# Optimization experiments

Hardware: AMD Instinct MI355X
Metric: run time of the kernel (lower is better)

Reference implementation:

```python
import jax, jax.numpy as jnp
import numpy as np


def setup_inputs() -> dict:
    key = jax.random.key(0)
    ks = jax.random.split(key, 4)
    N, T, D, H = 64, 512, 1024, 1024
    x = jax.random.normal(ks[0], (N, T, D), dtype=jnp.float32)
    h0 = jax.random.normal(ks[1], (N, H), dtype=jnp.float32)
    Wx = jax.random.normal(ks[2], (D, 4 * H), dtype=jnp.float32) / np.sqrt(D)
    Wh = jax.random.normal(ks[3], (H, 4 * H), dtype=jnp.float32) / np.sqrt(H)
    b = jnp.zeros((4 * H,), dtype=jnp.float32)
    return {"x": x, "h0": h0, "Wx": Wx, "Wh": Wh, "b": b}


def reference(x, h0, Wx, Wh, b):
    # x: [N, T, D]; h0: [N, H]; Wx: [D, 4H]; Wh: [H, 4H]; b: [4H]
    H = h0.shape[1]
    # Batch the input-to-hidden matmul over all timesteps at once: [N, T, 4H]
    xW = jnp.einsum('ntd,df->ntf', x, Wx) + b
    c0 = jnp.zeros_like(h0)

    def step(carry, xw_t):
        prev_h, prev_c = carry
        preact = xw_t + prev_h @ Wh           # [N, 4H]
        ai, af, ao, ag = jnp.split(preact, 4, axis=1)
        i = jax.nn.sigmoid(ai)
        f = jax.nn.sigmoid(af)
        o = jax.nn.sigmoid(ao)
        g = jnp.tanh(ag)
        next_c = f * prev_c + i * g
        next_h = o * jnp.tanh(next_c)
        return (next_h, next_c), next_h

    # scan over time: move T to leading axis
    _, hs = jax.lax.scan(step, (h0, c0), jnp.swapaxes(xW, 0, 1))
    return jnp.swapaxes(hs, 0, 1)  # [N, T, H]
```

## Files before the change

kernel.cpp:

```cpp
#include <hip/hip_runtime.h>
#include <cstdint>
#include <cstddef>

#define N_ 64
#define T_ 512
#define D_ 1024
#define H_ 1024
#define FH 4096

typedef __attribute__((ext_vector_type(8))) short bf16x8;
typedef __attribute__((ext_vector_type(4))) float f32x4;

static __device__ __forceinline__ uint16_t f2bf_(float f) {
  union { float f; uint32_t u; } v; v.f = f;
  uint32_t u = v.u + 0x7FFFu + ((v.u >> 16) & 1u);
  return (uint16_t)(u >> 16);
}
static __device__ __forceinline__ float bf2f_(uint16_t s) {
  union { uint32_t u; float f; } v; v.u = ((uint32_t)s) << 16;
  return v.f;
}
static __device__ __forceinline__ void unpk2_(unsigned long long e,
                                              uint32_t& hi, uint32_t& lo) {
  uint32_t a = (uint32_t)e, b = (uint32_t)(e >> 32);
  hi = (a >> 16) | (b & 0xFFFF0000u);
  lo = (a & 0xFFFFu) | (b << 16);
}

#define ALD(p) (*(p))

__global__ __launch_bounds__(256) void pack_w_k(const float* __restrict__ W,
                                                ushort* __restrict__ hi,
                                                ushort* __restrict__ lo) {
  const int i = blockIdx.x * 256 + threadIdx.x;
  const int lane = i & 63, kc = (i >> 6) & 31, bid = i >> 11;
  const int c = lane & 15;
  const int col = (c >> 2) * H_ + (bid << 2) + (c & 3);
  const int k0 = (kc << 5) + ((lane >> 4) << 3);
  const size_t o = ((size_t)(bid * 32 + kc) * 64 + lane) * 8;
#pragma unroll
  for (int e = 0; e < 8; ++e) {
    float v = W[(size_t)(k0 + e) * FH + col];
    ushort h = f2bf_(v);
    hi[o + e] = h;
    lo[o + e] = f2bf_(v - bf2f_(h));
  }
}

__global__ __launch_bounds__(256) void split_f32_k(const float* __restrict__ src,
                                                   ushort* __restrict__ hi,
                                                   ushort* __restrict__ lo,
                                                   unsigned* bar) {
  if (bar != nullptr && blockIdx.x == 0) {
    bar[threadIdx.x] = 0u;
    bar[256 + threadIdx.x] = 0u;
  }
  const size_t i = (size_t)blockIdx.x * 256 + threadIdx.x;
  float4 v = reinterpret_cast<const float4*>(src)[i];
  ushort4 h, l;
  h.x = f2bf_(v.x); l.x = f2bf_(v.x - bf2f_(h.x));
  h.y = f2bf_(v.y); l.y = f2bf_(v.y - bf2f_(h.y));
  h.z = f2bf_(v.z); l.z = f2bf_(v.z - bf2f_(h.z));
  h.w = f2bf_(v.w); l.w = f2bf_(v.w - bf2f_(h.w));
  reinterpret_cast<ushort4*>(hi)[i] = h;
  reinterpret_cast<ushort4*>(lo)[i] = l;
}

__global__ __launch_bounds__(256) void conv_h0pk_k(const float* __restrict__ src,
                                                   uint32_t* __restrict__ dst) {
  const int i = blockIdx.x * 256 + threadIdx.x;
  float4 v = reinterpret_cast<const float4*>(src)[i];
  uint4 o;
  { ushort h = f2bf_(v.x); o.x = ((uint32_t)h << 16) | f2bf_(v.x - bf2f_(h)); }
  { ushort h = f2bf_(v.y); o.y = ((uint32_t)h << 16) | f2bf_(v.y - bf2f_(h)); }
  { ushort h = f2bf_(v.z); o.z = ((uint32_t)h << 16) | f2bf_(v.z - bf2f_(h)); }
  { ushort h = f2bf_(v.w); o.w = ((uint32_t)h << 16) | f2bf_(v.w - bf2f_(h)); }
  reinterpret_cast<uint4*>(dst)[i] = o;
}

__global__ __launch_bounds__(512, 2) void lstm_persist_mfma(
    const ushort* __restrict__ Whh_g, const ushort* __restrict__ Whl_g,
    const ushort* __restrict__ Wxh, const ushort* __restrict__ Wxl,
    const ushort* __restrict__ xh, const ushort* __restrict__ xl,
    const float* __restrict__ bias,
    uint32_t* __restrict__ hseq,
    float* __restrict__ out, unsigned* __restrict__ bar) {
  extern __shared__ char ldsraw[];
  bf16x8* const WhH = (bf16x8*)ldsraw;
  bf16x8* const WhL = WhH + 2048;
  float* const pre = (float*)(WhL + 2048);
  float (*const xwr)[64][4][4] =
      (float(*)[64][4][4])(pre + 64 * 17);

  const int tid = threadIdx.x, bid = blockIdx.x;
  const int lane = tid & 63, w = tid >> 6;
  const int mt = w & 3;
  const int arow = (mt << 4) | (lane & 15);
  const int kg = lane >> 4;
  const int dc = lane & 15, dr = (lane >> 4) << 2;
  const int en = tid >> 2, ejj = tid & 3;

  unsigned* const rel = bar + 384;

  float bias4[4] = {0.f, 0.f, 0.f, 0.f};
  float creg = 0.f;
  if (tid < 256) {
#pragma unroll
    for (int g = 0; g < 4; ++g) bias4[g] = bias[g * H_ + (bid << 2) + ejj];
  }

  {
    const bf16x8* gh = reinterpret_cast<const bf16x8*>(Whh_g) + (size_t)bid * 2048;
    const bf16x8* gl = reinterpret_cast<const bf16x8*>(Whl_g) + (size_t)bid * 2048;
#pragma unroll
    for (int r = 0; r < 4; ++r) {
      int u = tid + (r << 9);
      WhH[u] = gh[u];
      WhL[u] = gl[u];
    }
  }
  __syncthreads();

  const bf16x8* Bxh = reinterpret_cast<const bf16x8*>(Wxh) + (size_t)bid * 2048 + lane;
  const bf16x8* Bxl = reinterpret_cast<const bf16x8*>(Wxl) + (size_t)bid * 2048 + lane;

  auto xburst = [&](int tb) {
    f32x4 xa0 = {0.f, 0.f, 0.f, 0.f};
    f32x4 xa1 = {0.f, 0.f, 0.f, 0.f};
    f32x4 xa2 = {0.f, 0.f, 0.f, 0.f};
    f32x4 xa3 = {0.f, 0.f, 0.f, 0.f};
    const ushort* axh = xh + ((size_t)arow * T_ + tb) * D_ + (kg << 3);
    const ushort* axl = xl + ((size_t)arow * T_ + tb) * D_ + (kg << 3);
#pragma unroll 4
    for (int kc = 0; kc < 32; ++kc) {
      bf16x8 bh = Bxh[kc << 6];
      bf16x8 bl = Bxl[kc << 6];
      bf16x8 a0h = *reinterpret_cast<const bf16x8*>(axh + (kc << 5));
      bf16x8 a0l = *reinterpret_cast<const bf16x8*>(axl + (kc << 5));
      bf16x8 a1h = *reinterpret_cast<const bf16x8*>(axh + D_ + (kc << 5));
      bf16x8 a1l = *reinterpret_cast<const bf16x8*>(axl + D_ + (kc << 5));
      bf16x8 a2h = *reinterpret_cast<const bf16x8*>(axh + 2 * D_ + (kc << 5));
      bf16x8 a2l = *reinterpret_cast<const bf16x8*>(axl + 2 * D_ + (kc << 5));
      bf16x8 a3h = *reinterpret_cast<const bf16x8*>(axh + 3 * D_ + (kc << 5));
      bf16x8 a3l = *reinterpret_cast<const bf16x8*>(axl + 3 * D_ + (kc << 5));
      xa0 = __builtin_amdgcn_mfma_f32_16x16x32_bf16(a0h, bh, xa0, 0, 0, 0);
      xa1 = __builtin_amdgcn_mfma_f32_16x16x32_bf16(a1h, bh, xa1, 0, 0, 0);
      xa2 = __builtin_amdgcn_mfma_f32_16x16x32_bf16(a2h, bh, xa2, 0, 0, 0);
      xa3 = __builtin_amdgcn_mfma_f32_16x16x32_bf16(a3h, bh, xa3, 0, 0, 0);
      xa0 = __builtin_amdgcn_mfma_f32_16x16x32_bf16(a0h, bl, xa0, 0, 0, 0);
      xa1 = __builtin_amdgcn_mfma_f32_16x16x32_bf16(a1h, bl, xa1, 0, 0, 0);
      xa2 = __builtin_amdgcn_mfma_f32_16x16x32_bf16(a2h, bl, xa2, 0, 0, 0);
      xa3 = __builtin_amdgcn_mfma_f32_16x16x32_bf16(a3h, bl, xa3, 0, 0, 0);
      xa0 = __builtin_amdgcn_mfma_f32_16x16x32_bf16(a0l, bh, xa0, 0, 0, 0);
      xa1 = __builtin_amdgcn_mfma_f32_16x16x32_bf16(a1l, bh, xa1, 0, 0, 0);
      xa2 = __builtin_amdgcn_mfma_f32_16x16x32_bf16(a2l, bh, xa2, 0, 0, 0);
      xa3 = __builtin_amdgcn_mfma_f32_16x16x32_bf16(a3l, bh, xa3, 0, 0, 0);
    }
    const int g = dc >> 2, jj = dc & 3;
#pragma unroll
    for (int r = 0; r < 4; ++r) {
      const int row = (mt << 4) + dr + r;
      xwr[(tb + 0) & 7][row][jj][g] = xa0[r];
      xwr[(tb + 1) & 7][row][jj][g] = xa1[r];
      xwr[(tb + 2) & 7][row][jj][g] = xa2[r];
      xwr[(tb + 3) & 7][row][jj][g] = xa3[r];
    }
  };

  if (w >= 4) {
    xburst(0);
    xburst(4);
  }

  for (int t = 0; t < T_; ++t) {
    if (w < 4) {
      f32x4 acc0 = {0.f, 0.f, 0.f, 0.f};
      f32x4 acc1 = {0.f, 0.f, 0.f, 0.f};
      const unsigned long long* Apk =
          (const unsigned long long*)(hseq + (size_t)t * 65536) +
          arow * 512 + kg * 4;

      unsigned long long pa0, pa1, pa2, pa3, pb0, pb1, pb2, pb3;
      unsigned long long pc0, pc1, pc2, pc3, pd0, pd1, pd2, pd3;
      unsigned long long qa0, qa1, qa2, qa3, qb0, qb1, qb2, qb3;
      unsigned long long qc0, qc1, qc2, qc3, qd0, qd1, qd2, qd3;

#define HLD(P, CH)                                                            \
  {                                                                           \
    const unsigned long long* ap_ = Apk + ((CH) << 6);                        \
    P##a0 = ALD(ap_ + 0);  P##a1 = ALD(ap_ + 1);                              \
    P##a2 = ALD(ap_ + 2);  P##a3 = ALD(ap_ + 3);                              \
    P##b0 = ALD(ap_ + 16); P##b1 = ALD(ap_ + 17);                             \
    P##b2 = ALD(ap_ + 18); P##b3 = ALD(ap_ + 19);                             \
    P##c0 = ALD(ap_ + 32); P##c1 = ALD(ap_ + 33);                             \
    P##c2 = ALD(ap_ + 34); P##c3 = ALD(ap_ + 35);                             \
    P##d0 = ALD(ap_ + 48); P##d1 = ALD(ap_ + 49);                             \
    P##d2 = ALD(ap_ + 50); P##d3 = ALD(ap_ + 51);                             \
  }

#define HKC(E0, E1, E2, E3, KCG, ACC)                                         \
  {                                                                           \
    union { uint32_t u[4]; bf16x8 v; } fh_, fl_;                              \
    unpk2_(E0, fh_.u[0], fl_.u[0]);                                           \
    unpk2_(E1, fh_.u[1], fl_.u[1]);                                           \
    unpk2_(E2, fh_.u[2], fl_.u[2]);                                           \
    unpk2_(E3, fh_.u[3], fl_.u[3]);                                           \
    bf16x8 bh_ = WhH[((KCG) << 6) + lane];                                    \
    bf16x8 bl_ = WhL[((KCG) << 6) + lane];                                    \
    ACC = __builtin_amdgcn_mfma_f32_16x16x32_bf16(fh_.v, bh_, ACC, 0, 0, 0);  \
    ACC = __builtin_amdgcn_mfma_f32_16x16x32_bf16(fh_.v, bl_, ACC, 0, 0, 0);  \
    ACC = __builtin_amdgcn_mfma_f32_16x16x32_bf16(fl_.v, bh_, ACC, 0, 0, 0);  \
  }

#define HCOMP(P, CH)                                                          \
  HKC(P##a0, P##a1, P##a2, P##a3, (CH) * 4 + 0, acc0)                         \
  HKC(P##b0, P##b1, P##b2, P##b3, (CH) * 4 + 1, acc1)                         \
  HKC(P##c0, P##c1, P##c2, P##c3, (CH) * 4 + 2, acc0)                         \
  HKC(P##d0, P##d1, P##d2, P##d3, (CH) * 4 + 3, acc1)

      HLD(p, 0)
      HLD(q, 1) HCOMP(p, 0)
      HLD(p, 2) HCOMP(q, 1)
      HLD(q, 3) HCOMP(p, 2)
      HLD(p, 4) HCOMP(q, 3)
      HLD(q, 5) HCOMP(p, 4)
      HLD(p, 6) HCOMP(q, 5)
      HLD(q, 7) HCOMP(p, 6)
      HCOMP(q, 7)
#undef HLD
#undef HKC
#undef HCOMP

      f32x4 accs = acc0 + acc1;
#pragma unroll
      for (int r = 0; r < 4; ++r)
        pre[((mt << 4) + dr + r) * 17 + dc] = accs[r];
    } else {
      if (t != 0 && (t & 3) == 0 && t + 4 < T_) xburst(t + 4);
    }
    __syncthreads();

    if (tid < 256) {
      const float* xvp = &xwr[t & 7][en][ejj][0];
      float a[4];
#pragma unroll
      for (int g = 0; g < 4; ++g)
        a[g] = pre[en * 17 + (g << 2) + ejj] + xvp[g] + bias4[g];
      float iv = 1.f / (1.f + __expf(-a[0]));
      float fv = 1.f / (1.f + __expf(-a[1]));
      float ov = 1.f / (1.f + __expf(-a[2]));
      float gv = tanhf(a[3]);
      creg = fmaf(fv, creg, iv * gv);
      float hn = ov * tanhf(creg);
      out[(size_t)en * ((size_t)T_ * H_) + (size_t)t * H_ + (bid << 2) + ejj] = hn;
      ushort hh = f2bf_(hn);
      uint32_t pk = ((uint32_t)hh << 16) | f2bf_(hn - bf2f_(hh));
      __hip_atomic_store(&hseq[(size_t)(t + 1) * 65536 + en * H_ + (bid << 2) + ejj],
                         pk, __ATOMIC_RELAXED, __HIP_MEMORY_SCOPE_AGENT);
    }

    asm volatile("s_waitcnt vmcnt(0)" ::: "memory");
    __syncthreads();

    const unsigned tgt = (unsigned)(t + 1);
    if (tid == 0)
      __hip_atomic_store(&bar[bid], tgt, __ATOMIC_RELAXED,
                         __HIP_MEMORY_SCOPE_AGENT);
    if (bid == 0 && tid < 64) {
      const unsigned long long* fl = (const unsigned long long*)bar;
      for (;;) {
        unsigned long long v0 = __hip_atomic_load(fl + tid, __ATOMIC_RELAXED,
                                                  __HIP_MEMORY_SCOPE_AGENT);
        unsigned long long v1 = __hip_atomic_load(fl + 64 + tid, __ATOMIC_RELAXED,
                                                  __HIP_MEMORY_SCOPE_AGENT);
        bool ok = ((unsigned)v0 >= tgt) && ((unsigned)(v0 >> 32) >= tgt) &&
                  ((unsigned)v1 >= tgt) && ((unsigned)(v1 >> 32) >= tgt);
        if (__all((int)ok)) break;
      }
      if (tid == 0)
        __hip_atomic_store(rel, tgt, __ATOMIC_RELAXED, __HIP_MEMORY_SCOPE_AGENT);
    }
    if (tid == 0) {
      while (__hip_atomic_load(rel, __ATOMIC_RELAXED,
                               __HIP_MEMORY_SCOPE_AGENT) < tgt)
        __builtin_amdgcn_s_sleep(1);
    }
    __syncthreads();
  }
}

__global__ __launch_bounds__(256) void lstm_step_fb(
    const float* __restrict__ xt, const float* __restrict__ Wx,
    const float* __restrict__ Wh, const float* __restrict__ bias,
    const float* __restrict__ h_prev, long long hstride,
    float* __restrict__ cbuf, float* __restrict__ h_out, int first) {
  __shared__ float hS[32][128];
  __shared__ float wT[32][132];
  __shared__ float pre[32][34];
  const int tid = threadIdx.x;
  const int colblk = blockIdx.x & 127;
  const int nh = blockIdx.x >> 7;
  const int j0 = colblk << 3;
  const int n0 = nh << 5;
  const int ng = tid >> 4, cg2 = tid & 15;
  const int na = ng << 1, ca = cg2 << 1;

  float acc[2][2] = {{0.f, 0.f}, {0.f, 0.f}};

#pragma unroll
  for (int pr = 0; pr < 2; ++pr) {
    const float* src = (pr == 0) ? h_prev : xt;
    long long sstr = (pr == 0) ? hstride : (long long)T_ * D_;
    const float* W = (pr == 0) ? Wh : Wx;
    for (int k0 = 0; k0 < 1024; k0 += 128) {
      __syncthreads();
#pragma unroll
      for (int p = 0; p < 4; ++p) {
        int idx = tid + (p << 8);
        int r = idx >> 5, c4 = (idx & 31) << 2;
        *reinterpret_cast<float4*>(&hS[r][c4]) =
            *reinterpret_cast<const float4*>(src + (size_t)(n0 + r) * sstr + k0 + c4);
      }
#pragma unroll
      for (int p = 0; p < 4; ++p) {
        int idx = tid + (p << 8);
        int k = idx >> 3, sub = idx & 7;
        int g = sub >> 1, hf = (sub & 1) << 2;
        float4 v = *reinterpret_cast<const float4*>(
            W + (size_t)(k0 + k) * FH + g * H_ + j0 + hf);
        int cb = (g << 3) + hf;
        wT[cb][k] = v.x; wT[cb + 1][k] = v.y; wT[cb + 2][k] = v.z; wT[cb + 3][k] = v.w;
      }
      __syncthreads();
#pragma unroll
      for (int kk = 0; kk < 128; kk += 4) {
        float4 h0v = *reinterpret_cast<const float4*>(&hS[na][kk]);
        float4 h1v = *reinterpret_cast<const float4*>(&hS[na + 1][kk]);
        float4 w0 = *reinterpret_cast<const float4*>(&wT[ca][kk]);
        float4 w1 = *reinterpret_cast<const float4*>(&wT[ca + 1][kk]);
        acc[0][0] = fmaf(h0v.x, w0.x, acc[0][0]); acc[0][0] = fmaf(h0v.y, w0.y, acc[0][0]);
        acc[0][0] = fmaf(h0v.z, w0.z, acc[0][0]); acc[0][0] = fmaf(h0v.w, w0.w, acc[0][0]);
        acc[0][1] = fmaf(h0v.x, w1.x, acc[0][1]); acc[0][1] = fmaf(h0v.y, w1.y, acc[0][1]);
        acc[0][1] = fmaf(h0v.z, w1.z, acc[0][1]); acc[0][1] = fmaf(h0v.w, w1.w, acc[0][1]);
        acc[1][0] = fmaf(h1v.x, w0.x, acc[1][0]); acc[1][0] = fmaf(h1v.y, w0.y, acc[1][0]);
        acc[1][0] = fmaf(h1v.z, w0.z, acc[1][0]); acc[1][0] = fmaf(h1v.w, w0.w, acc[1][0]);
        acc[1][1] = fmaf(h1v.x, w1.x, acc[1][1]); acc[1][1] = fmaf(h1v.y, w1.y, acc[1][1]);
        acc[1][1] = fmaf(h1v.z, w1.z, acc[1][1]); acc[1][1] = fmaf(h1v.w, w1.w, acc[1][1]);
      }
    }
  }

  pre[na][ca] = acc[0][0];
  pre[na][ca + 1] = acc[0][1];
  pre[na + 1][ca] = acc[1][0];
  pre[na + 1][ca + 1] = acc[1][1];
  __syncthreads();

  const int nl = tid >> 3, jl = tid & 7;
  const int n = n0 + nl;
  const int jg = j0 + jl;
  float ai = pre[nl][jl] + bias[jg];
  float af = pre[nl][8 + jl] + bias[H_ + jg];
  float ao = pre[nl][16 + jl] + bias[2 * H_ + jg];
  float ag = pre[nl][24 + jl] + bias[3 * H_ + jg];
  float cp = first ? 0.0f : cbuf[n * H_ + jg];
  float iv = 1.f / (1.f + __expf(-ai));
  float fv = 1.f / (1.f + __expf(-af));
  float ov = 1.f / (1.f + __expf(-ao));
  float gv = tanhf(ag);
  float cn = fmaf(fv, cp, iv * gv);
  cbuf[n * H_ + jg] = cn;
  h_out[(size_t)n * ((size_t)T_ * H_) + jg] = ov * tanhf(cn);
}

extern "C" void kernel_launch(void* const* d_in, const int* in_sizes, int n_in,
                              void* d_out, int out_size, void* d_ws, size_t ws_size,
                              hipStream_t stream) {
  (void)in_sizes; (void)n_in; (void)out_size;
  const float* x  = (const float*)d_in[0];
  const float* h0 = (const float*)d_in[1];
  const float* Wx = (const float*)d_in[2];
  const float* Wh = (const float*)d_in[3];
  const float* b  = (const float*)d_in[4];
  float* out = (float*)d_out;

  const size_t MB = 1u << 20;
  char* p = (char*)d_ws;

  if (ws_size >= 300 * MB) {
    unsigned* bar = (unsigned*)p;
    ushort* Whh = (ushort*)(p + 1 * MB);
    ushort* Whl = (ushort*)(p + 9 * MB);
    ushort* Wxh = (ushort*)(p + 17 * MB);
    ushort* Wxl = (ushort*)(p + 25 * MB);
    uint32_t* hseq = (uint32_t*)(p + 33 * MB);
    ushort* xh = (ushort*)(p + 168 * MB);
    ushort* xl = (ushort*)(p + 232 * MB);

    pack_w_k<<<dim3(2048), dim3(256), 0, stream>>>(Wh, Whh, Whl);
    pack_w_k<<<dim3(2048), dim3(256), 0, stream>>>(Wx, Wxh, Wxl);
    split_f32_k<<<dim3(32768), dim3(256), 0, stream>>>(x, xh, xl, bar);
    conv_h0pk_k<<<dim3(64), dim3(256), 0, stream>>>(h0, hseq);

    const unsigned SH = 65536 + 64 * 17 * 4 + 8 * 64 * 16 * 4;
    hipFuncSetAttribute((const void*)lstm_persist_mfma,
                        hipFuncAttributeMaxDynamicSharedMemorySize, (int)SH);
    lstm_persist_mfma<<<dim3(256), dim3(512), SH, stream>>>(
        Whh, Whl, Wxh, Wxl, xh, xl, b, hseq, out, bar);
  } else {
    float* cbuf = (float*)p;
    for (int t = 0; t < T_; ++t) {
      const float* hp = (t == 0) ? h0 : out + (size_t)(t - 1) * H_;
      long long hstr = (t == 0) ? (long long)H_ : (long long)T_ * H_;
      lstm_step_fb<<<dim3(256), dim3(256), 0, stream>>>(
          x + (size_t)t * D_, Wx, Wh, b, hp, hstr, cbuf,
          out + (size_t)t * H_, t == 0);
    }
  }
}
```

Baseline: 9.308 ms.

## Split recurrent K across all eight waves and overlap x-projection with barrier wait

All eight waves now compute the recurrent h@Wh product, each half of the waves taking half of the K dimension, and the two partial sums are combined through a doubled LDS pre buffer. The input projection burst is also split across all waves (two timesteps each) and moved to after the barrier arrive, so it fills the time spent waiting on the grid barrier. Launch bounds drop to one block per CU, which allows more registers. This is meant to shorten the serial per-step critical path, at the cost of extra LDS traffic and a possibly longer barrier wait when an x burst runs.

```diff
diff --git a/kernel.cpp b/kernel.cpp
--- a/kernel.cpp
+++ b/kernel.cpp
@@ -78,7 +78,7 @@
   reinterpret_cast<uint4*>(dst)[i] = o;
 }
 
-__global__ __launch_bounds__(512, 2) void lstm_persist_mfma(
+__global__ __launch_bounds__(512, 1) void lstm_persist_mfma(
     const ushort* __restrict__ Whh_g, const ushort* __restrict__ Whl_g,
     const ushort* __restrict__ Wxh, const ushort* __restrict__ Wxl,
     const ushort* __restrict__ xh, const ushort* __restrict__ xl,
@@ -90,11 +90,12 @@
   bf16x8* const WhL = WhH + 2048;
   float* const pre = (float*)(WhL + 2048);
   float (*const xwr)[64][4][4] =
-      (float(*)[64][4][4])(pre + 64 * 17);
+      (float(*)[64][4][4])(pre + 128 * 17);
 
   const int tid = threadIdx.x, bid = blockIdx.x;
   const int lane = tid & 63, w = tid >> 6;
-  const int mt = w & 3;
+  const int mt = w & 3, kh = w >> 2;
+  const int khb = kh << 4;
   const int arow = (mt << 4) | (lane & 15);
   const int kg = lane >> 4;
   const int dc = lane & 15, dr = (lane >> 4) << 2;
@@ -125,60 +126,50 @@
   const bf16x8* Bxl = reinterpret_cast<const bf16x8*>(Wxl) + (size_t)bid * 2048 + lane;
 
   auto xburst = [&](int tb) {
+    const int mt2 = mt;
+    const int t0 = tb + (kh << 1);
+    const int t1 = t0 + 1;
+    const int row = (mt2 << 4) | (lane & 15);
+    const ushort* a0h = xh + ((size_t)row * T_ + t0) * D_ + (kg << 3);
+    const ushort* a0l = xl + ((size_t)row * T_ + t0) * D_ + (kg << 3);
+    const ushort* a1h = xh + ((size_t)row * T_ + t1) * D_ + (kg << 3);
+    const ushort* a1l = xl + ((size_t)row * T_ + t1) * D_ + (kg << 3);
     f32x4 xa0 = {0.f, 0.f, 0.f, 0.f};
     f32x4 xa1 = {0.f, 0.f, 0.f, 0.f};
-    f32x4 xa2 = {0.f, 0.f, 0.f, 0.f};
-    f32x4 xa3 = {0.f, 0.f, 0.f, 0.f};
-    const ushort* axh = xh + ((size_t)arow * T_ + tb) * D_ + (kg << 3);
-    const ushort* axl = xl + ((size_t)arow * T_ + tb) * D_ + (kg << 3);
 #pragma unroll 4
     for (int kc = 0; kc < 32; ++kc) {
       bf16x8 bh = Bxh[kc << 6];
       bf16x8 bl = Bxl[kc << 6];
-      bf16x8 a0h = *reinterpret_cast<const bf16x8*>(axh + (kc << 5));
-      bf16x8 a0l = *reinterpret_cast<const bf16x8*>(axl + (kc << 5));
-      bf16x8 a1h = *reinterpret_cast<const bf16x8*>(axh + D_ + (kc << 5));
-      bf16x8 a1l = *reinterpret_cast<const bf16x8*>(axl + D_ + (kc << 5));
-      bf16x8 a2h = *reinterpret_cast<const bf16x8*>(axh + 2 * D_ + (kc << 5));
-      bf16x8 a2l = *reinterpret_cast<const bf16x8*>(axl + 2 * D_ + (kc << 5));
-      bf16x8 a3h = *reinterpret_cast<const bf16x8*>(axh + 3 * D_ + (kc << 5));
-      bf16x8 a3l = *reinterpret_cast<const bf16x8*>(axl + 3 * D_ + (kc << 5));
-      xa0 = __builtin_amdgcn_mfma_f32_16x16x32_bf16(a0h, bh, xa0, 0, 0, 0);
-      xa1 = __builtin_amdgcn_mfma_f32_16x16x32_bf16(a1h, bh, xa1, 0, 0, 0);
-      xa2 = __builtin_amdgcn_mfma_f32_16x16x32_bf16(a2h, bh, xa2, 0, 0, 0);
-      xa3 = __builtin_amdgcn_mfma_f32_16x16x32_bf16(a3h, bh, xa3, 0, 0, 0);
-      xa0 = __builtin_amdgcn_mfma_f32_16x16x32_bf16(a0h, bl, xa0, 0, 0, 0);
-      xa1 = __builtin_amdgcn_mfma_f32_16x16x32_bf16(a1h, bl, xa1, 0, 0, 0);
-      xa2 = __builtin_amdgcn_mfma_f32_16x16x32_bf16(a2h, bl, xa2, 0, 0, 0);
-      xa3 = __builtin_amdgcn_mfma_f32_16x16x32_bf16(a3h, bl, xa3, 0, 0, 0);
-      xa0 = __builtin_amdgcn_mfma_f32_16x16x32_bf16(a0l, bh, xa0, 0, 0, 0);
-      xa1 = __builtin_amdgcn_mfma_f32_16x16x32_bf16(a1l, bh, xa1, 0, 0, 0);
-      xa2 = __builtin_amdgcn_mfma_f32_16x16x32_bf16(a2l, bh, xa2, 0, 0, 0);
-      xa3 = __builtin_amdgcn_mfma_f32_16x16x32_bf16(a3l, bh, xa3, 0, 0, 0);
+      bf16x8 h0 = *reinterpret_cast<const bf16x8*>(a0h + (kc << 5));
+      bf16x8 l0 = *reinterpret_cast<const bf16x8*>(a0l + (kc << 5));
+      bf16x8 h1 = *reinterpret_cast<const bf16x8*>(a1h + (kc << 5));
+      bf16x8 l1 = *reinterpret_cast<const bf16x8*>(a1l + (kc << 5));
+      xa0 = __builtin_amdgcn_mfma_f32_16x16x32_bf16(h0, bh, xa0, 0, 0, 0);
+      xa1 = __builtin_amdgcn_mfma_f32_16x16x32_bf16(h1, bh, xa1, 0, 0, 0);
+      xa0 = __builtin_amdgcn_mfma_f32_16x16x32_bf16(h0, bl, xa0, 0, 0, 0);
+      xa1 = __builtin_amdgcn_mfma_f32_16x16x32_bf16(h1, bl, xa1, 0, 0, 0);
+      xa0 = __builtin_amdgcn_mfma_f32_16x16x32_bf16(l0, bh, xa0, 0, 0, 0);
+      xa1 = __builtin_amdgcn_mfma_f32_16x16x32_bf16(l1, bh, xa1, 0, 0, 0);
     }
     const int g = dc >> 2, jj = dc & 3;
 #pragma unroll
     for (int r = 0; r < 4; ++r) {
-      const int row = (mt << 4) + dr + r;
-      xwr[(tb + 0) & 7][row][jj][g] = xa0[r];
-      xwr[(tb + 1) & 7][row][jj][g] = xa1[r];
-      xwr[(tb + 2) & 7][row][jj][g] = xa2[r];
-      xwr[(tb + 3) & 7][row][jj][g] = xa3[r];
+      const int rw = (mt2 << 4) + dr + r;
+      xwr[t0 & 7][rw][jj][g] = xa0[r];
+      xwr[t1 & 7][rw][jj][g] = xa1[r];
     }
   };
 
-  if (w >= 4) {
-    xburst(0);
-    xburst(4);
-  }
+  xburst(0);
+  xburst(4);
 
   for (int t = 0; t < T_; ++t) {
-    if (w < 4) {
+    {
       f32x4 acc0 = {0.f, 0.f, 0.f, 0.f};
       f32x4 acc1 = {0.f, 0.f, 0.f, 0.f};
       const unsigned long long* Apk =
           (const unsigned long long*)(hseq + (size_t)t * 65536) +
-          arow * 512 + kg * 4;
+          arow * 512 + kg * 4 + (kh << 8);
 
       unsigned long long pa0, pa1, pa2, pa3, pb0, pb1, pb2, pb3;
       unsigned long long pc0, pc1, pc2, pc3, pd0, pd1, pd2, pd3;
@@ -213,20 +204,16 @@
   }
 
 #define HCOMP(P, CH)                                                          \
-  HKC(P##a0, P##a1, P##a2, P##a3, (CH) * 4 + 0, acc0)                         \
-  HKC(P##b0, P##b1, P##b2, P##b3, (CH) * 4 + 1, acc1)                         \
-  HKC(P##c0, P##c1, P##c2, P##c3, (CH) * 4 + 2, acc0)                         \
-  HKC(P##d0, P##d1, P##d2, P##d3, (CH) * 4 + 3, acc1)
+  HKC(P##a0, P##a1, P##a2, P##a3, khb + (CH) * 4 + 0, acc0)                   \
+  HKC(P##b0, P##b1, P##b2, P##b3, khb + (CH) * 4 + 1, acc1)                   \
+  HKC(P##c0, P##c1, P##c2, P##c3, khb + (CH) * 4 + 2, acc0)                   \
+  HKC(P##d0, P##d1, P##d2, P##d3, khb + (CH) * 4 + 3, acc1)
 
       HLD(p, 0)
       HLD(q, 1) HCOMP(p, 0)
       HLD(p, 2) HCOMP(q, 1)
       HLD(q, 3) HCOMP(p, 2)
-      HLD(p, 4) HCOMP(q, 3)
-      HLD(q, 5) HCOMP(p, 4)
-      HLD(p, 6) HCOMP(q, 5)
-      HLD(q, 7) HCOMP(p, 6)
-      HCOMP(q, 7)
+      HCOMP(q, 3)
 #undef HLD
 #undef HKC
 #undef HCOMP
@@ -234,9 +221,7 @@
       f32x4 accs = acc0 + acc1;
 #pragma unroll
       for (int r = 0; r < 4; ++r)
-        pre[((mt << 4) + dr + r) * 17 + dc] = accs[r];
-    } else {
-      if (t != 0 && (t & 3) == 0 && t + 4 < T_) xburst(t + 4);
+        pre[((kh << 6) + (mt << 4) + dr + r) * 17 + dc] = accs[r];
     }
     __syncthreads();
 
@@ -245,7 +230,8 @@
       float a[4];
 #pragma unroll
       for (int g = 0; g < 4; ++g)
-        a[g] = pre[en * 17 + (g << 2) + ejj] + xvp[g] + bias4[g];
+        a[g] = pre[en * 17 + (g << 2) + ejj] +
+               pre[(64 + en) * 17 + (g << 2) + ejj] + xvp[g] + bias4[g];
       float iv = 1.f / (1.f + __expf(-a[0]));
       float fv = 1.f / (1.f + __expf(-a[1]));
       float ov = 1.f / (1.f + __expf(-a[2]));
@@ -266,6 +252,9 @@
     if (tid == 0)
       __hip_atomic_store(&bar[bid], tgt, __ATOMIC_RELAXED,
                          __HIP_MEMORY_SCOPE_AGENT);
+
+    if (t != 0 && (t & 3) == 0 && t + 4 < T_) xburst(t + 4);
+
     if (bid == 0 && tid < 64) {
       const unsigned long long* fl = (const unsigned long long*)bar;
       for (;;) {
@@ -402,7 +391,7 @@
     split_f32_k<<<dim3(32768), dim3(256), 0, stream>>>(x, xh, xl, bar);
     conv_h0pk_k<<<dim3(64), dim3(256), 0, stream>>>(h0, hseq);
 
-    const unsigned SH = 65536 + 64 * 17 * 4 + 8 * 64 * 16 * 4;
+    const unsigned SH = 65536 + 128 * 17 * 4 + 8 * 64 * 16 * 4;
     hipFuncSetAttribute((const void*)lstm_persist_mfma,
                         hipFuncAttributeMaxDynamicSharedMemorySize, (int)SH);
     lstm_persist_mfma<<<dim3(256), dim3(512), SH, stream>>>(
```

Measured after the change: 9.110 ms. -2.1%, faster.
